# Optimization experiments

Hardware: AMD Instinct MI355X
Metric: run time of the kernel (lower is better)

Reference implementation:

```python
import jax, jax.numpy as jnp
import numpy as np

SLOT = 32
MLP_H = 128
N_SLOTS = 7
N_ITER = 3
EPS = 1e-8
SCALE = SLOT ** -0.5
LN_EPS = 1e-5  # torch LayerNorm default


def _ln(x, g, b):
    m = jnp.mean(x, axis=-1, keepdims=True)
    v = jnp.var(x, axis=-1, keepdims=True)
    return (x - m) * jax.lax.rsqrt(v + LN_EPS) * g + b


def setup_inputs() -> dict:
    key = jax.random.key(0)
    ks = jax.random.split(key, 16)
    def w(k, shape, fan_in):
        return jax.random.normal(k, shape, jnp.float32) * (1.0 / np.sqrt(fan_in))
    return {
        "inputs": jax.random.normal(ks[0], (64, 4096, MLP_H), jnp.float32),
        "slots_init": jax.random.normal(ks[1], (64, N_SLOTS, SLOT), jnp.float32),
        "ln_in_g": jnp.ones((MLP_H,), jnp.float32),
        "ln_in_b": jnp.zeros((MLP_H,), jnp.float32),
        "Wk": w(ks[2], (SLOT, MLP_H), MLP_H),
        "Wv": w(ks[3], (SLOT, MLP_H), MLP_H),
        "Wq": w(ks[4], (SLOT, SLOT), SLOT),
        "ln_s_g": jnp.ones((SLOT,), jnp.float32),
        "ln_s_b": jnp.zeros((SLOT,), jnp.float32),
        "gru_wi": w(ks[5], (3 * SLOT, SLOT), SLOT),
        "gru_wh": w(ks[6], (3 * SLOT, SLOT), SLOT),
        "gru_bi": jnp.zeros((3 * SLOT,), jnp.float32),
        "gru_bh": jnp.zeros((3 * SLOT,), jnp.float32),
        "ln_m_g": jnp.ones((SLOT,), jnp.float32),
        "ln_m_b": jnp.zeros((SLOT,), jnp.float32),
        "mlp_w1": w(ks[7], (MLP_H, SLOT), SLOT),
        "mlp_b1": jnp.zeros((MLP_H,), jnp.float32),
        "mlp_w2": w(ks[8], (SLOT, MLP_H), MLP_H),
        "mlp_b2": jnp.zeros((SLOT,), jnp.float32),
    }


def _gru_cell(x, h, wi, wh, bi, bh):
    # torch.nn.GRUCell math; gate order r, z, n
    gi = x @ wi.T + bi
    gh = h @ wh.T + bh
    gi_r, gi_z, gi_n = jnp.split(gi, 3, axis=-1)
    gh_r, gh_z, gh_n = jnp.split(gh, 3, axis=-1)
    r = jax.nn.sigmoid(gi_r + gh_r)
    z = jax.nn.sigmoid(gi_z + gh_z)
    n = jnp.tanh(gi_n + r * gh_n)
    return (1.0 - z) * n + z * h


def reference(inputs, slots_init, ln_in_g, ln_in_b, Wk, Wv, Wq, ln_s_g, ln_s_b,
              gru_wi, gru_wh, gru_bi, gru_bh, ln_m_g, ln_m_b,
              mlp_w1, mlp_b1, mlp_w2, mlp_b2):
    x = _ln(inputs, ln_in_g, ln_in_b)           # [B, N, 128]
    k = x @ Wk.T                                # [B, N, 32]
    v = x @ Wv.T                                # [B, N, 32]

    slots = slots_init                          # [B, S, 32]
    attn = None
    for m in range(N_ITER + 1):
        slots_prev = slots
        s = _ln(slots, ln_s_g, ln_s_b)
        q = s @ Wq.T                            # [B, S, 32]
        dots = jnp.einsum('bid,bjd->bij', q, k) * SCALE   # [B, S, N]
        attn = jax.nn.softmax(dots, axis=1) + EPS          # softmax over slots
        attn = attn / jnp.sum(attn, axis=-1, keepdims=True)
        updates = jnp.einsum('bjd,bij->bid', v, attn)      # [B, S, 32]
        slots = _gru_cell(updates, slots_prev, gru_wi, gru_wh, gru_bi, gru_bh)
        h = _ln(slots, ln_m_g, ln_m_b)
        h = jax.nn.relu(h @ mlp_w1.T + mlp_b1) @ mlp_w2.T + mlp_b2
        slots = slots + h
        if m == N_ITER - 1:
            slots = jax.lax.stop_gradient(slots)
    return slots, attn, slots
```

## Files before the change

### kernel.cpp

```cpp
#include <hip/hip_runtime.h>
#include <stdint.h>

#define B_   64
#define N_   4096
#define H_   128
#define S_   7
#define D_   32
#define SCALE_ 0.17677669529663687f
#define EPS_   1e-8f
#define LNEPS_ 1e-5f

typedef __bf16 bf16x8 __attribute__((ext_vector_type(8)));
typedef float  floatx4 __attribute__((ext_vector_type(4)));

__device__ __forceinline__ uint32_t cvt2(float a, float b){
  union { __bf16 h[2]; uint32_t u; } r;
  r.h[0] = (__bf16)a; r.h[1] = (__bf16)b;
  return r.u;
}
__device__ __forceinline__ float bfLO(uint32_t u){ union{uint32_t i; float f;} x; x.i = u << 16;         return x.f; }
__device__ __forceinline__ float bfHI(uint32_t u){ union{uint32_t i; float f;} x; x.i = u & 0xffff0000u; return x.f; }
__device__ __forceinline__ void up8(uint4 u, float* o){
  o[0]=bfLO(u.x); o[1]=bfHI(u.x); o[2]=bfLO(u.y); o[3]=bfHI(u.y);
  o[4]=bfLO(u.z); o[5]=bfHI(u.z); o[6]=bfLO(u.w); o[7]=bfHI(u.w);
}

__global__ __launch_bounds__(256) void init_w(const float* __restrict__ Wk, const float* __restrict__ Wv,
                                              const float* __restrict__ g,  const float* __restrict__ bta,
                                              uint16_t* __restrict__ fragbuf,
                                              float* __restrict__ c1arr, float* __restrict__ c2arr){
  int tid = blockIdx.x * 256 + threadIdx.x;
  if (blockIdx.x < 4){
    int nt = tid >> 8, kc = (tid >> 6) & 3, l = tid & 63;
    int col = (nt & 1) * 16 + (l & 15);
    int dbase = kc * 32 + (l >> 4) * 8;
    const float* wr = (nt < 2 ? Wk : Wv) + col * 128 + dbase;
    const float* gr = g + dbase;
    uint32_t u[4];
    #pragma unroll
    for (int j = 0; j < 4; ++j)
      u[j] = cvt2(wr[2*j] * gr[2*j], wr[2*j+1] * gr[2*j+1]);
    *reinterpret_cast<uint4*>(fragbuf + (size_t)tid * 8) = make_uint4(u[0], u[1], u[2], u[3]);
  } else {
    int t = threadIdx.x;
    if (t < 128){
      int which = t >> 5, col = t & 31;
      const float* Wb  = (which & 2) ? Wv : Wk;
      const float* vec = (which & 1) ? bta : g;
      float a = 0.f;
      for (int d = 0; d < 128; ++d) a += vec[d] * Wb[col * 128 + d];
      float* dst = (which & 1) ? c2arr : c1arr;
      dst[(which >> 1) * 32 + col] = a;
    }
  }
}

__global__ __launch_bounds__(256) void ln_kv(const float* __restrict__ x,
                                             const uint16_t* __restrict__ fragbuf,
                                             const float* __restrict__ c1arr, const float* __restrict__ c2arr,
                                             uint16_t* __restrict__ kb, uint16_t* __restrict__ vb){
  __shared__ union {
    uint16_t atile[64 * 136];
    float    rep[4352];
  } sh;
  __shared__ float2 stats[32 * 65];
  __shared__ float2 rowstat[64];
  int t = threadIdx.x;
  int l = t & 63, w = t >> 6;
  size_t rowbase = (size_t)blockIdx.x * 64;

  bf16x8 bfr[4][4];
  #pragma unroll
  for (int nt = 0; nt < 4; ++nt)
    #pragma unroll
    for (int kc = 0; kc < 4; ++kc)
      bfr[nt][kc] = *reinterpret_cast<const bf16x8*>(fragbuf + (((nt * 4 + kc) * 64 + l) * 8));

  float c1c[4], c2c[4];
  #pragma unroll
  for (int nt = 0; nt < 4; ++nt){
    int colk = (nt & 1) * 16 + (l & 15);
    c1c[nt] = c1arr[(nt >> 1) * 32 + colk];
    c2c[nt] = c2arr[(nt >> 1) * 32 + colk];
  }

  const float4* xp = reinterpret_cast<const float4*>(x + rowbase * H_);
  #pragma unroll
  for (int k = 0; k < 8; ++k){
    float4 v = xp[k * 256 + t];
    int row = 8 * k + (t >> 5);
    uint32_t lo = cvt2(v.x, v.y);
    uint32_t hi = cvt2(v.z, v.w);
    *reinterpret_cast<uint2*>(&sh.atile[row * 136 + (t & 31) * 4]) = make_uint2(lo, hi);
    float s  = v.x + v.y + v.z + v.w;
    float s2 = v.x*v.x + v.y*v.y + v.z*v.z + v.w*v.w;
    stats[(t & 31) * 65 + row] = make_float2(s, s2);
  }
  __syncthreads();

  {
    int row = t >> 2, q = t & 3;
    float s = 0.f, s2 = 0.f;
    #pragma unroll
    for (int j = 0; j < 8; ++j){
      float2 p = stats[(q * 8 + j) * 65 + row];
      s += p.x; s2 += p.y;
    }
    s  += __shfl_xor(s, 1);  s2 += __shfl_xor(s2, 1);
    s  += __shfl_xor(s, 2);  s2 += __shfl_xor(s2, 2);
    if (q == 0){
      float mean = s * (1.f / 128.f);
      float var  = s2 * (1.f / 128.f) - mean * mean;
      float rstd = rsqrtf(var + LNEPS_);
      rowstat[row] = make_float2(rstd, -mean * rstd);
    }
  }
  __syncthreads();

  floatx4 acc[4] = {{0,0,0,0},{0,0,0,0},{0,0,0,0},{0,0,0,0}};
  #pragma unroll
  for (int kc = 0; kc < 4; ++kc){
    bf16x8 afr = *reinterpret_cast<const bf16x8*>(
        &sh.atile[(w * 16 + (l & 15)) * 136 + kc * 32 + (l >> 4) * 8]);
    #pragma unroll
    for (int nt = 0; nt < 4; ++nt)
      acc[nt] = __builtin_amdgcn_mfma_f32_16x16x32_bf16(afr, bfr[nt][kc], acc[nt], 0, 0, 0);
  }
  __syncthreads();

  #pragma unroll
  for (int j = 0; j < 4; ++j){
    int rloc = w * 16 + (l >> 4) * 4 + j;
    float2 ab = rowstat[rloc];
    #pragma unroll
    for (int nt = 0; nt < 4; ++nt){
      int base = (nt < 2) ? 0 : 2176;
      int gc = (nt & 1) * 16 + (l & 15);
      sh.rep[base + rloc * 34 + gc] = fmaf(ab.x, acc[nt][j], fmaf(ab.y, c1c[nt], c2c[nt]));
    }
  }
  __syncthreads();

  uint32_t* kout = reinterpret_cast<uint32_t*>(kb + rowbase * 32);
  uint32_t* vout = reinterpret_cast<uint32_t*>(vb + rowbase * 32);
  #pragma unroll
  for (int it = 0; it < 4; ++it){
    int lin = it * 256 + t;
    int row = lin >> 4, wd = (lin & 15) * 2;
    kout[lin] = cvt2(sh.rep[row * 34 + wd],        sh.rep[row * 34 + wd + 1]);
    vout[lin] = cvt2(sh.rep[2176 + row * 34 + wd], sh.rep[2176 + row * 34 + wd + 1]);
  }
}

__global__ __launch_bounds__(256) void attn_acc(const uint16_t* __restrict__ kb, const uint16_t* __restrict__ vb,
                                                const float* __restrict__ qbuf,
                                                float* __restrict__ updbuf, float* __restrict__ rowsumbuf,
                                                float* __restrict__ aub, int lastIter){
  __shared__ float au[S_ * 257];
  __shared__ float vtile[256 * 32];
  int b = blockIdx.y, chunk = blockIdx.x, t = threadIdx.x;

  int rem = t % 56, prt = t / 56;
  int pi = rem >> 3, pc4 = rem & 7;

  float rs[7];
  #pragma unroll
  for (int i = 0; i < 7; ++i) rs[i] = 0.f;
  float ux = 0.f, uy = 0.f, uz = 0.f, uw = 0.f;

  const float* qb = qbuf + b * (S_ * D_);

  for (int tile = 0; tile < 2; ++tile){
    int j = chunk * 512 + tile * 256 + t;
    const uint4* kr = reinterpret_cast<const uint4*>(kb + ((size_t)b * N_ + j) * 32);
    float kf[32];
    #pragma unroll
    for (int p = 0; p < 4; ++p) up8(kr[p], kf + p * 8);

    float dv[7];
    #pragma unroll
    for (int i = 0; i < 7; ++i){
      const float* qr = qb + i * 32;
      float a = 0.f;
      #pragma unroll
      for (int c = 0; c < 32; ++c) a += qr[c] * kf[c];
      dv[i] = a * SCALE_;
    }
    float mx = dv[0];
    #pragma unroll
    for (int i = 1; i < 7; ++i) mx = fmaxf(mx, dv[i]);
    float p[7]; float sum = 0.f;
    #pragma unroll
    for (int i = 0; i < 7; ++i){ p[i] = __expf(dv[i] - mx); sum += p[i]; }
    float inv = 1.f / sum;
    #pragma unroll
    for (int i = 0; i < 7; ++i){
      p[i] = p[i] * inv + EPS_;
      rs[i] += p[i];
      au[i * 257 + t] = p[i];
    }
    if (lastIter){
      #pragma unroll
      for (int i = 0; i < 7; ++i) aub[(size_t)(b * S_ + i) * N_ + j] = p[i];
    }
    const uint4* vr = reinterpret_cast<const uint4*>(vb + ((size_t)b * N_ + j) * 32);
    float vf[32];
    #pragma unroll
    for (int p = 0; p < 4; ++p) up8(vr[p], vf + p * 8);
    #pragma unroll
    for (int q4 = 0; q4 < 8; ++q4){
      int blk = q4 ^ (t & 7);
      float4 vv = make_float4(vf[q4*4], vf[q4*4+1], vf[q4*4+2], vf[q4*4+3]);
      *reinterpret_cast<float4*>(&vtile[t * 32 + blk * 4]) = vv;
    }
    __syncthreads();

    if (t < 224){
      const float* aur = au + pi * 257 + prt * 64;
      #pragma unroll 4
      for (int jj0 = 0; jj0 < 64; ++jj0){
        int jj = prt * 64 + jj0;
        float a = aur[jj0];
        int blk = pc4 ^ (jj & 7);
        float4 vv = *reinterpret_cast<const float4*>(&vtile[jj * 32 + blk * 4]);
        ux += a * vv.x; uy += a * vv.y; uz += a * vv.z; uw += a * vv.w;
      }
    }
    __syncthreads();
  }

  #pragma unroll
  for (int i = 0; i < 7; ++i) au[i * 257 + t] = rs[i];
  __syncthreads();
  for (int off = 128; off >= 1; off >>= 1){
    if (t < off){
      #pragma unroll
      for (int i = 0; i < 7; ++i) au[i * 257 + t] += au[i * 257 + t + off];
    }
    __syncthreads();
  }
  if (t < 7) atomicAdd(&rowsumbuf[b * S_ + t], au[t * 257]);
  if (t < 224){
    float* up = updbuf + (size_t)(b * S_ + pi) * 32 + pc4 * 4;
    atomicAdd(up + 0, ux); atomicAdd(up + 1, uy);
    atomicAdd(up + 2, uz); atomicAdd(up + 3, uw);
  }
}

__global__ __launch_bounds__(256) void slot_update(
    const float* __restrict__ slots_init,
    float* __restrict__ slotsbuf, float* __restrict__ updbuf, float* __restrict__ rowsumbuf,
    float* __restrict__ qbuf,
    const float* __restrict__ Wq,
    const float* __restrict__ lnsg, const float* __restrict__ lnsb,
    const float* __restrict__ gwi, const float* __restrict__ gwh,
    const float* __restrict__ gbi, const float* __restrict__ gbh,
    const float* __restrict__ lnmg, const float* __restrict__ lnmb,
    const float* __restrict__ w1, const float* __restrict__ b1,
    const float* __restrict__ w2, const float* __restrict__ b2,
    float* __restrict__ out0, float* __restrict__ out2,
    int doC, int doA, int isFinal)
{
  int b = blockIdx.x, t = threadIdx.x;
  int i = t >> 5, c = t & 31;
  __shared__ float sPrev[224], sU[224], sNew[224], sT[224], hM[896];
  float snew = 0.f;

  if (doC){
    if (t < 224){
      sPrev[t] = slotsbuf[b * 224 + t];
      sU[t] = updbuf[b * 224 + t] / rowsumbuf[b * S_ + i];
    }
    __syncthreads();
    if (t < 224){
      float gi[3], gh[3];
      #pragma unroll
      for (int x3 = 0; x3 < 3; ++x3){
        int gg = x3 * 32 + c;
        float ai = gbi[gg], ah = gbh[gg];
        #pragma unroll
        for (int d = 0; d < 32; ++d){
          ai += sU[i * 32 + d]    * gwi[gg * 32 + d];
          ah += sPrev[i * 32 + d] * gwh[gg * 32 + d];
        }
        gi[x3] = ai; gh[x3] = ah;
      }
      float r = 1.f / (1.f + __expf(-(gi[0] + gh[0])));
      float z = 1.f / (1.f + __expf(-(gi[1] + gh[1])));
      float n = tanhf(gi[2] + r * gh[2]);
      snew = (1.f - z) * n + z * sPrev[t];
      sNew[t] = snew;
    }
    __syncthreads();
    if (t < 224){
      float mu = 0.f, sq = 0.f;
      #pragma unroll
      for (int d = 0; d < 32; ++d){ float v = sNew[i * 32 + d]; mu += v; sq += v * v; }
      mu *= (1.f / 32.f);
      float var = sq * (1.f / 32.f) - mu * mu;
      float rstd = rsqrtf(var + LNEPS_);
      sT[t] = (snew - mu) * rstd * lnmg[c] + lnmb[c];
    }
    __syncthreads();
    if (t < 224){
      #pragma unroll
      for (int kk = 0; kk < 4; ++kk){
        int hc = c + kk * 32;
        float a = b1[hc];
        #pragma unroll
        for (int d = 0; d < 32; ++d) a += sT[i * 32 + d] * w1[hc * 32 + d];
        hM[i * 128 + hc] = fmaxf(a, 0.f);
      }
    }
    __syncthreads();
    if (t < 224){
      float a0 = 0.f, a1 = 0.f, a2 = 0.f, a3 = 0.f;
      for (int hh = 0; hh < 128; hh += 4){
        a0 += hM[i * 128 + hh    ] * w2[c * 128 + hh    ];
        a1 += hM[i * 128 + hh + 1] * w2[c * 128 + hh + 1];
        a2 += hM[i * 128 + hh + 2] * w2[c * 128 + hh + 2];
        a3 += hM[i * 128 + hh + 3] * w2[c * 128 + hh + 3];
      }
      snew = snew + b2[c] + ((a0 + a1) + (a2 + a3));
      slotsbuf[b * 224 + t] = snew;
      if (isFinal){ out0[b * 224 + t] = snew; out2[b * 224 + t] = snew; }
      sNew[t] = snew;
    }
  } else {
    if (t < 224){
      snew = slots_init[b * 224 + t];
      slotsbuf[b * 224 + t] = snew;
      sNew[t] = snew;
    }
  }

  if (doA){
    __syncthreads();
    if (t < 224){
      float mu = 0.f, sq = 0.f;
      #pragma unroll
      for (int d = 0; d < 32; ++d){ float v = sNew[i * 32 + d]; mu += v; sq += v * v; }
      mu *= (1.f / 32.f);
      float var = sq * (1.f / 32.f) - mu * mu;
      float rstd = rsqrtf(var + LNEPS_);
      sT[t] = (snew - mu) * rstd * lnsg[c] + lnsb[c];
    }
    __syncthreads();
    if (t < 224){
      float a = 0.f;
      #pragma unroll
      for (int d = 0; d < 32; ++d) a += sT[i * 32 + d] * Wq[c * 32 + d];
      qbuf[b * 224 + t] = a;
      updbuf[b * 224 + t] = 0.f;
    }
    if (t < 7) rowsumbuf[b * S_ + t] = 0.f;
  }
}

__global__ __launch_bounds__(256) void attn_final(const float* __restrict__ aub,
                                                  const float* __restrict__ rowsumbuf,
                                                  float* __restrict__ out1){
  int idx = blockIdx.x * 256 + threadIdx.x;
  int bi = idx >> 12;
  out1[idx] = aub[idx] / rowsumbuf[bi];
}

extern "C" void kernel_launch(void* const* d_in, const int* in_sizes, int n_in,
                              void* d_out, int out_size, void* d_ws, size_t ws_size,
                              hipStream_t stream)
{
  (void)in_sizes; (void)n_in; (void)out_size; (void)ws_size;
  const float* inp   = (const float*)d_in[0];
  const float* sini  = (const float*)d_in[1];
  const float* lng   = (const float*)d_in[2];
  const float* lnb   = (const float*)d_in[3];
  const float* Wk    = (const float*)d_in[4];
  const float* Wv    = (const float*)d_in[5];
  const float* Wq    = (const float*)d_in[6];
  const float* lnsg  = (const float*)d_in[7];
  const float* lnsb  = (const float*)d_in[8];
  const float* gwi   = (const float*)d_in[9];
  const float* gwh   = (const float*)d_in[10];
  const float* gbi   = (const float*)d_in[11];
  const float* gbh   = (const float*)d_in[12];
  const float* lnmg  = (const float*)d_in[13];
  const float* lnmb  = (const float*)d_in[14];
  const float* w1    = (const float*)d_in[15];
  const float* b1    = (const float*)d_in[16];
  const float* w2    = (const float*)d_in[17];
  const float* b2    = (const float*)d_in[18];

  char* w = (char*)d_ws;
  uint16_t* kbuf   = (uint16_t*)w; w += (size_t)B_ * N_ * 32 * 2;
  uint16_t* vbuf   = (uint16_t*)w; w += (size_t)B_ * N_ * 32 * 2;
  float* qbuf      = (float*)w; w += B_ * 224 * 4;
  float* slotsbuf  = (float*)w; w += B_ * 224 * 4;
  float* updbuf    = (float*)w; w += B_ * 224 * 4;
  float* rowsumbuf = (float*)w; w += B_ * S_ * 4;
  float* aubuf     = (float*)w; w += (size_t)B_ * S_ * N_ * 4;
  uint16_t* fragbuf= (uint16_t*)w; w += 8192 * 2;
  float* c1arr     = (float*)w; w += 64 * 4;
  float* c2arr     = (float*)w; w += 64 * 4;

  float* out0 = (float*)d_out;
  float* out1 = out0 + B_ * S_ * D_;
  float* out2 = out1 + B_ * S_ * N_;

  hipLaunchKernelGGL(init_w, dim3(5), dim3(256), 0, stream, Wk, Wv, lng, lnb, fragbuf, c1arr, c2arr);
  hipLaunchKernelGGL(ln_kv, dim3(4096), dim3(256), 0, stream, inp, fragbuf, c1arr, c2arr, kbuf, vbuf);

  hipLaunchKernelGGL(slot_update, dim3(64), dim3(256), 0, stream,
                     sini, slotsbuf, updbuf, rowsumbuf, qbuf, Wq, lnsg, lnsb,
                     gwi, gwh, gbi, gbh, lnmg, lnmb, w1, b1, w2, b2,
                     out0, out2, 0, 1, 0);

  for (int m = 0; m < 4; ++m){
    hipLaunchKernelGGL(attn_acc, dim3(8, 64), dim3(256), 0, stream,
                       kbuf, vbuf, qbuf, updbuf, rowsumbuf, aubuf, (m == 3) ? 1 : 0);
    hipLaunchKernelGGL(slot_update, dim3(64), dim3(256), 0, stream,
                       sini, slotsbuf, updbuf, rowsumbuf, qbuf, Wq, lnsg, lnsb,
                       gwi, gwh, gbi, gbh, lnmg, lnmb, w1, b1, w2, b2,
                       out0, out2, 1, (m < 3) ? 1 : 0, (m == 3) ? 1 : 0);
  }

  hipLaunchKernelGGL(attn_final, dim3((B_ * S_ * N_) / 256), dim3(256), 0, stream,
                     aubuf, rowsumbuf, out1);
}
```

Baseline: 185.7 us.

## Fuse slot update into attention kernel via last-block atomic counter

```diff
diff --git a/kernel.cpp b/kernel.cpp
--- a/kernel.cpp
+++ b/kernel.cpp
@@ -6,6 +6,7 @@
 #define H_   128
 #define S_   7
 #define D_   32
+#define NCH_ 16
 #define SCALE_ 0.17677669529663687f
 #define EPS_   1e-8f
 #define LNEPS_ 1e-5f
@@ -28,9 +29,16 @@
 __global__ __launch_bounds__(256) void init_w(const float* __restrict__ Wk, const float* __restrict__ Wv,
                                               const float* __restrict__ g,  const float* __restrict__ bta,
                                               uint16_t* __restrict__ fragbuf,
-                                              float* __restrict__ c1arr, float* __restrict__ c2arr){
-  int tid = blockIdx.x * 256 + threadIdx.x;
+                                              float* __restrict__ c1arr, float* __restrict__ c2arr,
+                                              const float* __restrict__ sini,
+                                              float* __restrict__ slotsbuf, float* __restrict__ qbuf,
+                                              float* __restrict__ updbuf, float* __restrict__ rowsumbuf,
+                                              int* __restrict__ cnt,
+                                              const float* __restrict__ Wq,
+                                              const float* __restrict__ lnsg, const float* __restrict__ lnsb){
+  int t = threadIdx.x;
   if (blockIdx.x < 4){
+    int tid = blockIdx.x * 256 + t;
     int nt = tid >> 8, kc = (tid >> 6) & 3, l = tid & 63;
     int col = (nt & 1) * 16 + (l & 15);
     int dbase = kc * 32 + (l >> 4) * 8;
@@ -41,8 +49,7 @@
     for (int j = 0; j < 4; ++j)
       u[j] = cvt2(wr[2*j] * gr[2*j], wr[2*j+1] * gr[2*j+1]);
     *reinterpret_cast<uint4*>(fragbuf + (size_t)tid * 8) = make_uint4(u[0], u[1], u[2], u[3]);
-  } else {
-    int t = threadIdx.x;
+  } else if (blockIdx.x == 4){
     if (t < 128){
       int which = t >> 5, col = t & 31;
       const float* Wb  = (which & 2) ? Wv : Wk;
@@ -52,6 +59,35 @@
       float* dst = (which & 1) ? c2arr : c1arr;
       dst[(which >> 1) * 32 + col] = a;
     }
+  } else {
+    int b = blockIdx.x - 5;
+    int i = t >> 5, c = t & 31;
+    __shared__ float sNew[224], sT[224];
+    if (t < 224){
+      float s = sini[b * 224 + t];
+      slotsbuf[b * 224 + t] = s;
+      sNew[t] = s;
+      updbuf[b * 224 + t] = 0.f;
+    }
+    if (t < 7) rowsumbuf[b * S_ + t] = 0.f;
+    if (t < 4) cnt[t * 64 + b] = 0;
+    __syncthreads();
+    if (t < 224){
+      float mu = 0.f, sq = 0.f;
+      #pragma unroll
+      for (int d = 0; d < 32; ++d){ float v = sNew[i * 32 + d]; mu += v; sq += v * v; }
+      mu *= (1.f / 32.f);
+      float var = sq * (1.f / 32.f) - mu * mu;
+      float rstd = rsqrtf(var + LNEPS_);
+      sT[t] = (sNew[t] - mu) * rstd * lnsg[c] + lnsb[c];
+    }
+    __syncthreads();
+    if (t < 224){
+      float a = 0.f;
+      #pragma unroll
+      for (int d = 0; d < 32; ++d) a += sT[i * 32 + d] * Wq[c * 32 + d];
+      qbuf[b * 224 + t] = a;
+    }
   }
 }
 
@@ -63,25 +99,24 @@
     uint16_t atile[64 * 136];
     float    rep[4352];
   } sh;
-  __shared__ float2 stats[32 * 65];
+  __shared__ float2 stats[64 * 8];
   __shared__ float2 rowstat[64];
   int t = threadIdx.x;
   int l = t & 63, w = t >> 6;
+  int half = w >> 1;
+  int r0 = (w & 1) * 32;
   size_t rowbase = (size_t)blockIdx.x * 64;
 
-  bf16x8 bfr[4][4];
+  bf16x8 bfr[2][4];
+  float c1c[2], c2c[2];
   #pragma unroll
-  for (int nt = 0; nt < 4; ++nt)
+  for (int n2 = 0; n2 < 2; ++n2){
     #pragma unroll
     for (int kc = 0; kc < 4; ++kc)
-      bfr[nt][kc] = *reinterpret_cast<const bf16x8*>(fragbuf + (((nt * 4 + kc) * 64 + l) * 8));
-
-  float c1c[4], c2c[4];
-  #pragma unroll
-  for (int nt = 0; nt < 4; ++nt){
-    int colk = (nt & 1) * 16 + (l & 15);
-    c1c[nt] = c1arr[(nt >> 1) * 32 + colk];
-    c2c[nt] = c2arr[(nt >> 1) * 32 + colk];
+      bfr[n2][kc] = *reinterpret_cast<const bf16x8*>(fragbuf + ((((half*2+n2) * 4 + kc) * 64 + l) * 8));
+    int colk = n2 * 16 + (l & 15);
+    c1c[n2] = c1arr[half * 32 + colk];
+    c2c[n2] = c2arr[half * 32 + colk];
   }
 
   const float4* xp = reinterpret_cast<const float4*>(x + rowbase * H_);
@@ -94,275 +129,272 @@
     *reinterpret_cast<uint2*>(&sh.atile[row * 136 + (t & 31) * 4]) = make_uint2(lo, hi);
     float s  = v.x + v.y + v.z + v.w;
     float s2 = v.x*v.x + v.y*v.y + v.z*v.z + v.w*v.w;
-    stats[(t & 31) * 65 + row] = make_float2(s, s2);
-  }
-  __syncthreads();
-
-  {
-    int row = t >> 2, q = t & 3;
-    float s = 0.f, s2 = 0.f;
-    #pragma unroll
-    for (int j = 0; j < 8; ++j){
-      float2 p = stats[(q * 8 + j) * 65 + row];
-      s += p.x; s2 += p.y;
-    }
     s  += __shfl_xor(s, 1);  s2 += __shfl_xor(s2, 1);
     s  += __shfl_xor(s, 2);  s2 += __shfl_xor(s2, 2);
-    if (q == 0){
-      float mean = s * (1.f / 128.f);
-      float var  = s2 * (1.f / 128.f) - mean * mean;
-      float rstd = rsqrtf(var + LNEPS_);
-      rowstat[row] = make_float2(rstd, -mean * rstd);
-    }
-  }
-  __syncthreads();
-
-  floatx4 acc[4] = {{0,0,0,0},{0,0,0,0},{0,0,0,0},{0,0,0,0}};
+    if ((t & 3) == 0) stats[row * 8 + ((t & 31) >> 2)] = make_float2(s, s2);
+  }
+  __syncthreads();
+
+  if (t < 64){
+    float s = 0.f, s2 = 0.f;
+    #pragma unroll
+    for (int jx = 0; jx < 8; ++jx){
+      float2 p = stats[t * 8 + jx];
+      s += p.x; s2 += p.y;
+    }
+    float mean = s * (1.f / 128.f);
+    float var  = s2 * (1.f / 128.f) - mean * mean;
+    float rstd = rsqrtf(var + LNEPS_);
+    rowstat[t] = make_float2(rstd, -mean * rstd);
+  }
+  __syncthreads();
+
+  floatx4 acc[2][2] = {{{0,0,0,0},{0,0,0,0}},{{0,0,0,0},{0,0,0,0}}};
   #pragma unroll
   for (int kc = 0; kc < 4; ++kc){
-    bf16x8 afr = *reinterpret_cast<const bf16x8*>(
-        &sh.atile[(w * 16 + (l & 15)) * 136 + kc * 32 + (l >> 4) * 8]);
-    #pragma unroll
-    for (int nt = 0; nt < 4; ++nt)
-      acc[nt] = __builtin_amdgcn_mfma_f32_16x16x32_bf16(afr, bfr[nt][kc], acc[nt], 0, 0, 0);
-  }
-  __syncthreads();
-
+    bf16x8 afr0 = *reinterpret_cast<const bf16x8*>(
+        &sh.atile[(r0 +      (l & 15)) * 136 + kc * 32 + (l >> 4) * 8]);
+    bf16x8 afr1 = *reinterpret_cast<const bf16x8*>(
+        &sh.atile[(r0 + 16 + (l & 15)) * 136 + kc * 32 + (l >> 4) * 8]);
+    #pragma unroll
+    for (int n2 = 0; n2 < 2; ++n2){
+      acc[0][n2] = __builtin_amdgcn_mfma_f32_16x16x32_bf16(afr0, bfr[n2][kc], acc[0][n2], 0, 0, 0);
+      acc[1][n2] = __builtin_amdgcn_mfma_f32_16x16x32_bf16(afr1, bfr[n2][kc], acc[1][n2], 0, 0, 0);
+    }
+  }
+  __syncthreads();
+
+  int base = half * 2176;
   #pragma unroll
-  for (int j = 0; j < 4; ++j){
-    int rloc = w * 16 + (l >> 4) * 4 + j;
-    float2 ab = rowstat[rloc];
-    #pragma unroll
-    for (int nt = 0; nt < 4; ++nt){
-      int base = (nt < 2) ? 0 : 2176;
-      int gc = (nt & 1) * 16 + (l & 15);
-      sh.rep[base + rloc * 34 + gc] = fmaf(ab.x, acc[nt][j], fmaf(ab.y, c1c[nt], c2c[nt]));
-    }
-  }
-  __syncthreads();
-
-  uint32_t* kout = reinterpret_cast<uint32_t*>(kb + rowbase * 32);
-  uint32_t* vout = reinterpret_cast<uint32_t*>(vb + rowbase * 32);
-  #pragma unroll
-  for (int it = 0; it < 4; ++it){
-    int lin = it * 256 + t;
-    int row = lin >> 4, wd = (lin & 15) * 2;
-    kout[lin] = cvt2(sh.rep[row * 34 + wd],        sh.rep[row * 34 + wd + 1]);
-    vout[lin] = cvt2(sh.rep[2176 + row * 34 + wd], sh.rep[2176 + row * 34 + wd + 1]);
-  }
-}
-
-__global__ __launch_bounds__(256) void attn_acc(const uint16_t* __restrict__ kb, const uint16_t* __restrict__ vb,
-                                                const float* __restrict__ qbuf,
-                                                float* __restrict__ updbuf, float* __restrict__ rowsumbuf,
-                                                float* __restrict__ aub, int lastIter){
-  __shared__ float au[S_ * 257];
-  __shared__ float vtile[256 * 32];
-  int b = blockIdx.y, chunk = blockIdx.x, t = threadIdx.x;
-
-  int rem = t % 56, prt = t / 56;
-  int pi = rem >> 3, pc4 = rem & 7;
-
-  float rs[7];
-  #pragma unroll
-  for (int i = 0; i < 7; ++i) rs[i] = 0.f;
-  float ux = 0.f, uy = 0.f, uz = 0.f, uw = 0.f;
-
-  const float* qb = qbuf + b * (S_ * D_);
-
-  for (int tile = 0; tile < 2; ++tile){
-    int j = chunk * 512 + tile * 256 + t;
-    const uint4* kr = reinterpret_cast<const uint4*>(kb + ((size_t)b * N_ + j) * 32);
-    float kf[32];
-    #pragma unroll
-    for (int p = 0; p < 4; ++p) up8(kr[p], kf + p * 8);
-
-    float dv[7];
-    #pragma unroll
-    for (int i = 0; i < 7; ++i){
-      const float* qr = qb + i * 32;
-      float a = 0.f;
-      #pragma unroll
-      for (int c = 0; c < 32; ++c) a += qr[c] * kf[c];
-      dv[i] = a * SCALE_;
-    }
-    float mx = dv[0];
-    #pragma unroll
-    for (int i = 1; i < 7; ++i) mx = fmaxf(mx, dv[i]);
-    float p[7]; float sum = 0.f;
-    #pragma unroll
-    for (int i = 0; i < 7; ++i){ p[i] = __expf(dv[i] - mx); sum += p[i]; }
-    float inv = 1.f / sum;
-    #pragma unroll
-    for (int i = 0; i < 7; ++i){
-      p[i] = p[i] * inv + EPS_;
-      rs[i] += p[i];
-      au[i * 257 + t] = p[i];
-    }
-    if (lastIter){
-      #pragma unroll
-      for (int i = 0; i < 7; ++i) aub[(size_t)(b * S_ + i) * N_ + j] = p[i];
-    }
-    const uint4* vr = reinterpret_cast<const uint4*>(vb + ((size_t)b * N_ + j) * 32);
-    float vf[32];
-    #pragma unroll
-    for (int p = 0; p < 4; ++p) up8(vr[p], vf + p * 8);
-    #pragma unroll
-    for (int q4 = 0; q4 < 8; ++q4){
-      int blk = q4 ^ (t & 7);
-      float4 vv = make_float4(vf[q4*4], vf[q4*4+1], vf[q4*4+2], vf[q4*4+3]);
-      *reinterpret_cast<float4*>(&vtile[t * 32 + blk * 4]) = vv;
-    }
-    __syncthreads();
-
-    if (t < 224){
-      const float* aur = au + pi * 257 + prt * 64;
-      #pragma unroll 4
-      for (int jj0 = 0; jj0 < 64; ++jj0){
-        int jj = prt * 64 + jj0;
-        float a = aur[jj0];
-        int blk = pc4 ^ (jj & 7);
-        float4 vv = *reinterpret_cast<const float4*>(&vtile[jj * 32 + blk * 4]);
-        ux += a * vv.x; uy += a * vv.y; uz += a * vv.z; uw += a * vv.w;
-      }
-    }
-    __syncthreads();
-  }
-
-  #pragma unroll
-  for (int i = 0; i < 7; ++i) au[i * 257 + t] = rs[i];
-  __syncthreads();
-  for (int off = 128; off >= 1; off >>= 1){
-    if (t < off){
-      #pragma unroll
-      for (int i = 0; i < 7; ++i) au[i * 257 + t] += au[i * 257 + t + off];
-    }
-    __syncthreads();
-  }
-  if (t < 7) atomicAdd(&rowsumbuf[b * S_ + t], au[t * 257]);
-  if (t < 224){
-    float* up = updbuf + (size_t)(b * S_ + pi) * 32 + pc4 * 4;
-    atomicAdd(up + 0, ux); atomicAdd(up + 1, uy);
-    atomicAdd(up + 2, uz); atomicAdd(up + 3, uw);
-  }
-}
-
-__global__ __launch_bounds__(256) void slot_update(
-    const float* __restrict__ slots_init,
-    float* __restrict__ slotsbuf, float* __restrict__ updbuf, float* __restrict__ rowsumbuf,
-    float* __restrict__ qbuf,
-    const float* __restrict__ Wq,
-    const float* __restrict__ lnsg, const float* __restrict__ lnsb,
+  for (int rt = 0; rt < 2; ++rt){
+    #pragma unroll
+    for (int j = 0; j < 4; ++j){
+      int rloc = r0 + rt * 16 + (l >> 4) * 4 + j;
+      float2 ab = rowstat[rloc];
+      #pragma unroll
+      for (int n2 = 0; n2 < 2; ++n2)
+        sh.rep[base + rloc * 34 + n2 * 16 + (l & 15)] =
+            fmaf(ab.x, acc[rt][n2][j], fmaf(ab.y, c1c[n2], c2c[n2]));
+    }
+  }
+  __syncthreads();
+
+  uint4* kout4 = reinterpret_cast<uint4*>(kb + rowbase * 32);
+  uint4* vout4 = reinterpret_cast<uint4*>(vb + rowbase * 32);
+  {
+    int row = t >> 2, w8 = t & 3;
+    const float* sk = &sh.rep[row * 34 + w8 * 8];
+    const float* sv = &sh.rep[2176 + row * 34 + w8 * 8];
+    kout4[t] = make_uint4(cvt2(sk[0],sk[1]), cvt2(sk[2],sk[3]), cvt2(sk[4],sk[5]), cvt2(sk[6],sk[7]));
+    vout4[t] = make_uint4(cvt2(sv[0],sv[1]), cvt2(sv[2],sv[3]), cvt2(sv[4],sv[5]), cvt2(sv[6],sv[7]));
+  }
+}
+
+__global__ __launch_bounds__(256) void attn_acc(
+    const uint16_t* __restrict__ kb, const uint16_t* __restrict__ vb,
+    float* __restrict__ qbuf, float* __restrict__ updbuf, float* __restrict__ rowsumbuf,
+    float* __restrict__ aubuf, int* __restrict__ cnt,
+    float* __restrict__ slotsbuf, float* __restrict__ invbuf,
     const float* __restrict__ gwi, const float* __restrict__ gwh,
     const float* __restrict__ gbi, const float* __restrict__ gbh,
     const float* __restrict__ lnmg, const float* __restrict__ lnmb,
     const float* __restrict__ w1, const float* __restrict__ b1,
     const float* __restrict__ w2, const float* __restrict__ b2,
-    float* __restrict__ out0, float* __restrict__ out2,
-    int doC, int doA, int isFinal)
+    const float* __restrict__ Wq, const float* __restrict__ lnsg, const float* __restrict__ lnsb,
+    float* __restrict__ out0, float* __restrict__ out2, int m)
 {
-  int b = blockIdx.x, t = threadIdx.x;
+  __shared__ float au[S_ * 257];
+  __shared__ union {
+    float vtile[256 * 32];
+    struct { float sPrev[224], sU[224], sNew[224], sT[224], hM[896]; } tl;
+  } shv;
+  __shared__ int winflag;
+  int b = blockIdx.y, chunk = blockIdx.x, t = threadIdx.x;
+  int j = chunk * 256 + t;
+
+  const float* qb = qbuf + b * (S_ * D_);
+  {
+    const uint4* kr = reinterpret_cast<const uint4*>(kb + ((size_t)b * N_ + j) * 32);
+    float kf[32];
+    #pragma unroll
+    for (int p = 0; p < 4; ++p) up8(kr[p], kf + p * 8);
+
+    float dv[7];
+    #pragma unroll
+    for (int i = 0; i < 7; ++i){
+      const float* qr = qb + i * 32;
+      float a = 0.f;
+      #pragma unroll
+      for (int c = 0; c < 32; ++c) a += qr[c] * kf[c];
+      dv[i] = a * SCALE_;
+    }
+    float mx = dv[0];
+    #pragma unroll
+    for (int i = 1; i < 7; ++i) mx = fmaxf(mx, dv[i]);
+    float p[7]; float sum = 0.f;
+    #pragma unroll
+    for (int i = 0; i < 7; ++i){ p[i] = __expf(dv[i] - mx); sum += p[i]; }
+    float inv = 1.f / sum;
+    #pragma unroll
+    for (int i = 0; i < 7; ++i){
+      p[i] = p[i] * inv + EPS_;
+      au[i * 257 + t] = p[i];
+    }
+    if (m == 3){
+      #pragma unroll
+      for (int i = 0; i < 7; ++i) aubuf[(size_t)(b * S_ + i) * N_ + j] = p[i];
+    }
+    const uint4* vr = reinterpret_cast<const uint4*>(vb + ((size_t)b * N_ + j) * 32);
+    float vf[32];
+    #pragma unroll
+    for (int p4 = 0; p4 < 4; ++p4) up8(vr[p4], vf + p4 * 8);
+    #pragma unroll
+    for (int q4 = 0; q4 < 8; ++q4){
+      int blk = q4 ^ (t & 7);
+      *reinterpret_cast<float4*>(&shv.vtile[t * 32 + blk * 4]) =
+          make_float4(vf[q4*4], vf[q4*4+1], vf[q4*4+2], vf[q4*4+3]);
+    }
+  }
+  __syncthreads();
+
+  int rem = t % 56, prt = t / 56;
+  int pi = rem >> 3, pc4 = rem & 7;
+  float ux = 0.f, uy = 0.f, uz = 0.f, uw = 0.f;
+  if (t < 224){
+    const float* aur = au + pi * 257 + prt * 64;
+    #pragma unroll 4
+    for (int jj0 = 0; jj0 < 64; ++jj0){
+      int jj = prt * 64 + jj0;
+      float a = aur[jj0];
+      int blk = pc4 ^ (jj & 7);
+      float4 vv = *reinterpret_cast<const float4*>(&shv.vtile[jj * 32 + blk * 4]);
+      ux += a * vv.x; uy += a * vv.y; uz += a * vv.z; uw += a * vv.w;
+    }
+  }
+  __syncthreads();
+
+  for (int off = 128; off >= 1; off >>= 1){
+    if (t < off){
+      #pragma unroll
+      for (int i = 0; i < 7; ++i) au[i * 257 + t] += au[i * 257 + t + off];
+    }
+    __syncthreads();
+  }
+  if (t < 7) atomicAdd(&rowsumbuf[b * S_ + t], au[t * 257]);
+  if (t < 224){
+    float* up = updbuf + (size_t)(b * S_ + pi) * 32 + pc4 * 4;
+    atomicAdd(up + 0, ux); atomicAdd(up + 1, uy);
+    atomicAdd(up + 2, uz); atomicAdd(up + 3, uw);
+  }
+  __syncthreads();
+
+  if (t == 0){
+    __threadfence();
+    int old = atomicAdd(&cnt[m * 64 + b], 1);
+    winflag = (old == NCH_ - 1);
+  }
+  __syncthreads();
+  if (!winflag) return;
+  if (t == 0){ cnt[m * 64 + b] = 0; __threadfence(); }
+  __syncthreads();
+
   int i = t >> 5, c = t & 31;
-  __shared__ float sPrev[224], sU[224], sNew[224], sT[224], hM[896];
   float snew = 0.f;
-
-  if (doC){
-    if (t < 224){
-      sPrev[t] = slotsbuf[b * 224 + t];
-      sU[t] = updbuf[b * 224 + t] / rowsumbuf[b * S_ + i];
-    }
-    __syncthreads();
-    if (t < 224){
-      float gi[3], gh[3];
-      #pragma unroll
-      for (int x3 = 0; x3 < 3; ++x3){
-        int gg = x3 * 32 + c;
-        float ai = gbi[gg], ah = gbh[gg];
-        #pragma unroll
-        for (int d = 0; d < 32; ++d){
-          ai += sU[i * 32 + d]    * gwi[gg * 32 + d];
-          ah += sPrev[i * 32 + d] * gwh[gg * 32 + d];
-        }
-        gi[x3] = ai; gh[x3] = ah;
+  if (t < 224){
+    float upv = atomicAdd(&updbuf[b * 224 + t], 0.f);
+    float rsv = atomicAdd(&rowsumbuf[b * S_ + i], 0.f);
+    shv.tl.sPrev[t] = slotsbuf[b * 224 + t];
+    shv.tl.sU[t] = upv / rsv;
+  }
+  __syncthreads();
+  if (t < 224) updbuf[b * 224 + t] = 0.f;
+  if (t < 7){
+    if (m == 3) invbuf[b * S_ + t] = 1.f / atomicAdd(&rowsumbuf[b * S_ + t], 0.f);
+    rowsumbuf[b * S_ + t] = 0.f;
+  }
+  if (t < 224){
+    float gi[3], gh[3];
+    #pragma unroll
+    for (int x3 = 0; x3 < 3; ++x3){
+      int gg = x3 * 32 + c;
+      float ai = gbi[gg], ah = gbh[gg];
+      #pragma unroll
+      for (int d = 0; d < 32; ++d){
+        ai += shv.tl.sU[i * 32 + d]    * gwi[gg * 32 + d];
+        ah += shv.tl.sPrev[i * 32 + d] * gwh[gg * 32 + d];
       }
-      float r = 1.f / (1.f + __expf(-(gi[0] + gh[0])));
-      float z = 1.f / (1.f + __expf(-(gi[1] + gh[1])));
-      float n = tanhf(gi[2] + r * gh[2]);
-      snew = (1.f - z) * n + z * sPrev[t];
-      sNew[t] = snew;
-    }
+      gi[x3] = ai; gh[x3] = ah;
+    }
+    float r = 1.f / (1.f + __expf(-(gi[0] + gh[0])));
+    float z = 1.f / (1.f + __expf(-(gi[1] + gh[1])));
+    float n = tanhf(gi[2] + r * gh[2]);
+    snew = (1.f - z) * n + z * shv.tl.sPrev[t];
+    shv.tl.sNew[t] = snew;
+  }
+  __syncthreads();
+  if (t < 224){
+    float mu = 0.f, sq = 0.f;
+    #pragma unroll
+    for (int d = 0; d < 32; ++d){ float v = shv.tl.sNew[i * 32 + d]; mu += v; sq += v * v; }
+    mu *= (1.f / 32.f);
+    float var = sq * (1.f / 32.f) - mu * mu;
+    float rstd = rsqrtf(var + LNEPS_);
+    shv.tl.sT[t] = (snew - mu) * rstd * lnmg[c] + lnmb[c];
+  }
+  __syncthreads();
+  if (t < 224){
+    #pragma unroll
+    for (int kk = 0; kk < 4; ++kk){
+      int hc = c + kk * 32;
+      float a = b1[hc];
+      #pragma unroll
+      for (int d = 0; d < 32; ++d) a += shv.tl.sT[i * 32 + d] * w1[hc * 32 + d];
+      shv.tl.hM[i * 128 + hc] = fmaxf(a, 0.f);
+    }
+  }
+  __syncthreads();
+  if (t < 224){
+    float a0 = 0.f, a1 = 0.f, a2 = 0.f, a3 = 0.f;
+    for (int hh = 0; hh < 128; hh += 4){
+      a0 += shv.tl.hM[i * 128 + hh    ] * w2[c * 128 + hh    ];
+      a1 += shv.tl.hM[i * 128 + hh + 1] * w2[c * 128 + hh + 1];
+      a2 += shv.tl.hM[i * 128 + hh + 2] * w2[c * 128 + hh + 2];
+      a3 += shv.tl.hM[i * 128 + hh + 3] * w2[c * 128 + hh + 3];
+    }
+    snew = snew + b2[c] + ((a0 + a1) + (a2 + a3));
+    slotsbuf[b * 224 + t] = snew;
+    if (m == 3){ out0[b * 224 + t] = snew; out2[b * 224 + t] = snew; }
+    shv.tl.sNew[t] = snew;
+  }
+  if (m < 3){
     __syncthreads();
     if (t < 224){
       float mu = 0.f, sq = 0.f;
       #pragma unroll
-      for (int d = 0; d < 32; ++d){ float v = sNew[i * 32 + d]; mu += v; sq += v * v; }
+      for (int d = 0; d < 32; ++d){ float v = shv.tl.sNew[i * 32 + d]; mu += v; sq += v * v; }
       mu *= (1.f / 32.f);
       float var = sq * (1.f / 32.f) - mu * mu;
       float rstd = rsqrtf(var + LNEPS_);
-      sT[t] = (snew - mu) * rstd * lnmg[c] + lnmb[c];
-    }
-    __syncthreads();
-    if (t < 224){
-      #pragma unroll
-      for (int kk = 0; kk < 4; ++kk){
-        int hc = c + kk * 32;
-        float a = b1[hc];
-        #pragma unroll
-        for (int d = 0; d < 32; ++d) a += sT[i * 32 + d] * w1[hc * 32 + d];
-        hM[i * 128 + hc] = fmaxf(a, 0.f);
-      }
-    }
-    __syncthreads();
-    if (t < 224){
-      float a0 = 0.f, a1 = 0.f, a2 = 0.f, a3 = 0.f;
-      for (int hh = 0; hh < 128; hh += 4){
-        a0 += hM[i * 128 + hh    ] * w2[c * 128 + hh    ];
-        a1 += hM[i * 128 + hh + 1] * w2[c * 128 + hh + 1];
-        a2 += hM[i * 128 + hh + 2] * w2[c * 128 + hh + 2];
-        a3 += hM[i * 128 + hh + 3] * w2[c * 128 + hh + 3];
-      }
-      snew = snew + b2[c] + ((a0 + a1) + (a2 + a3));
-      slotsbuf[b * 224 + t] = snew;
-      if (isFinal){ out0[b * 224 + t] = snew; out2[b * 224 + t] = snew; }
-      sNew[t] = snew;
-    }
-  } else {
-    if (t < 224){
-      snew = slots_init[b * 224 + t];
-      slotsbuf[b * 224 + t] = snew;
-      sNew[t] = snew;
-    }
-  }
-
-  if (doA){
-    __syncthreads();
-    if (t < 224){
-      float mu = 0.f, sq = 0.f;
-      #pragma unroll
-      for (int d = 0; d < 32; ++d){ float v = sNew[i * 32 + d]; mu += v; sq += v * v; }
-      mu *= (1.f / 32.f);
-      float var = sq * (1.f / 32.f) - mu * mu;
-      float rstd = rsqrtf(var + LNEPS_);
-      sT[t] = (snew - mu) * rstd * lnsg[c] + lnsb[c];
+      shv.tl.sT[t] = (shv.tl.sNew[t] - mu) * rstd * lnsg[c] + lnsb[c];
     }
     __syncthreads();
     if (t < 224){
       float a = 0.f;
       #pragma unroll
-      for (int d = 0; d < 32; ++d) a += sT[i * 32 + d] * Wq[c * 32 + d];
+      for (int d = 0; d < 32; ++d) a += shv.tl.sT[i * 32 + d] * Wq[c * 32 + d];
       qbuf[b * 224 + t] = a;
-      updbuf[b * 224 + t] = 0.f;
-    }
-    if (t < 7) rowsumbuf[b * S_ + t] = 0.f;
-  }
-}
-
-__global__ __launch_bounds__(256) void attn_final(const float* __restrict__ aub,
-                                                  const float* __restrict__ rowsumbuf,
+    }
+  }
+}
+
+__global__ __launch_bounds__(256) void attn_final(const float* __restrict__ aubuf,
+                                                  const float* __restrict__ invbuf,
                                                   float* __restrict__ out1){
-  int idx = blockIdx.x * 256 + threadIdx.x;
-  int bi = idx >> 12;
-  out1[idx] = aub[idx] / rowsumbuf[bi];
+  int idx4 = blockIdx.x * 256 + threadIdx.x;
+  int bi = idx4 >> 10;
+  float inv = invbuf[bi];
+  float4 a = reinterpret_cast<const float4*>(aubuf)[idx4];
+  reinterpret_cast<float4*>(out1)[idx4] = make_float4(a.x*inv, a.y*inv, a.z*inv, a.w*inv);
 }
 
 extern "C" void kernel_launch(void* const* d_in, const int* in_sizes, int n_in,
@@ -397,32 +429,30 @@
   float* slotsbuf  = (float*)w; w += B_ * 224 * 4;
   float* updbuf    = (float*)w; w += B_ * 224 * 4;
   float* rowsumbuf = (float*)w; w += B_ * S_ * 4;
+  float* invbuf    = (float*)w; w += B_ * S_ * 4;
   float* aubuf     = (float*)w; w += (size_t)B_ * S_ * N_ * 4;
   uint16_t* fragbuf= (uint16_t*)w; w += 8192 * 2;
   float* c1arr     = (float*)w; w += 64 * 4;
   float* c2arr     = (float*)w; w += 64 * 4;
+  int* cntbuf      = (int*)w;   w += 4 * 64 * 4;
 
   float* out0 = (float*)d_out;
   float* out1 = out0 + B_ * S_ * D_;
   float* out2 = out1 + B_ * S_ * N_;
 
-  hipLaunchKernelGGL(init_w, dim3(5), dim3(256), 0, stream, Wk, Wv, lng, lnb, fragbuf, c1arr, c2arr);
+  hipLaunchKernelGGL(init_w, dim3(69), dim3(256), 0, stream,
+                     Wk, Wv, lng, lnb, fragbuf, c1arr, c2arr,
+                     sini, slotsbuf, qbuf, updbuf, rowsumbuf, cntbuf, Wq, lnsg, lnsb);
   hipLaunchKernelGGL(ln_kv, dim3(4096), dim3(256), 0, stream, inp, fragbuf, c1arr, c2arr, kbuf, vbuf);
 
-  hipLaunchKernelGGL(slot_update, dim3(64), dim3(256), 0, stream,
-                     sini, slotsbuf, updbuf, rowsumbuf, qbuf, Wq, lnsg, lnsb,
-                     gwi, gwh, gbi, gbh, lnmg, lnmb, w1, b1, w2, b2,
-                     out0, out2, 0, 1, 0);
-
   for (int m = 0; m < 4; ++m){
-    hipLaunchKernelGGL(attn_acc, dim3(8, 64), dim3(256), 0, stream,
-                       kbuf, vbuf, qbuf, updbuf, rowsumbuf, aubuf, (m == 3) ? 1 : 0);
-    hipLaunchKernelGGL(slot_update, dim3(64), dim3(256), 0, stream,
-                       sini, slotsbuf, updbuf, rowsumbuf, qbuf, Wq, lnsg, lnsb,
+    hipLaunchKernelGGL(attn_acc, dim3(NCH_, 64), dim3(256), 0, stream,
+                       kbuf, vbuf, qbuf, updbuf, rowsumbuf, aubuf, cntbuf,
+                       slotsbuf, invbuf,
                        gwi, gwh, gbi, gbh, lnmg, lnmb, w1, b1, w2, b2,
-                       out0, out2, 1, (m < 3) ? 1 : 0, (m == 3) ? 1 : 0);
-  }
-
-  hipLaunchKernelGGL(attn_final, dim3((B_ * S_ * N_) / 256), dim3(256), 0, stream,
-                     aubuf, rowsumbuf, out1);
-}
+                       Wq, lnsg, lnsb, out0, out2, m);
+  }
+
+  hipLaunchKernelGGL(attn_final, dim3((B_ * S_ * N_) / 1024), dim3(256), 0, stream,
+                     aubuf, invbuf, out1);
+}
```

Measured after the change: 413.2 us. 2.23x slower.
